# Kernel tuning notes

Measured on AMD Instinct MI355X. Metric: run time of the kernel, lower is better.

## Reference

```python
import jax, jax.numpy as jnp
import numpy as np

N_LOC = 20000
N_EXP = 200000
H = 64
E = 1500000
L = 400000


def setup_inputs() -> dict:
    key = jax.random.key(0)
    ks = jax.random.split(key, 24)
    f = jnp.float32
    w = lambda k, shp: jax.random.normal(k, shp, dtype=f) * 0.1
    # edges: ('location','of','experts'): src in [0,N_LOC), dst in [0,N_EXP)
    src = jax.random.randint(ks[0], (E,), 0, N_LOC)
    dst = jax.random.randint(ks[1], (E,), 0, N_EXP)
    edge_of = jnp.stack([src, dst])          # location -> experts
    edge_rev = jnp.stack([dst, src])         # experts -> location (ToUndirected)
    row = jax.random.randint(ks[2], (L,), 0, N_LOC)
    col = jax.random.randint(ks[3], (L,), 0, N_EXP)
    edge_label_index = jnp.stack([row, col])
    return dict(
        emb_loc=w(ks[4], (N_LOC, H)), emb_exp=w(ks[5], (N_EXP, H)),
        W1l_of=w(ks[6], (H, H)), b1_of=jnp.zeros((H,), f), W1r_of=w(ks[7], (H, H)),
        W1l_rev=w(ks[8], (H, H)), b1_rev=jnp.zeros((H,), f), W1r_rev=w(ks[9], (H, H)),
        W2l_of=w(ks[10], (H, H)), b2_of=jnp.zeros((H,), f), W2r_of=w(ks[11], (H, H)),
        W2l_rev=w(ks[12], (H, H)), b2_rev=jnp.zeros((H,), f), W2r_rev=w(ks[13], (H, H)),
        dW1=w(ks[14], (2 * H, H)), db1=jnp.zeros((H,), f),
        dW2=w(ks[15], (H, 1)), db2=jnp.zeros((1,), f),
        edge_of=edge_of, edge_rev=edge_rev, edge_label_index=edge_label_index,
    )


def _sage(x_src, x_dst, edge, Wl, b, Wr, n_dst):
    # PyG SAGEConv: lin_l(mean of neighbor msgs) + lin_r(x_dst); bias only in lin_l
    s, d = edge[0], edge[1]
    msg = x_src[s]                                   # [E, H] gather
    summed = jax.ops.segment_sum(msg, d, num_segments=n_dst)
    cnt = jax.ops.segment_sum(jnp.ones((edge.shape[1],), x_src.dtype), d, num_segments=n_dst)
    agg = summed / jnp.maximum(cnt, 1.0)[:, None]
    return agg @ Wl + b + x_dst @ Wr


def reference(emb_loc, emb_exp,
              W1l_of, b1_of, W1r_of, W1l_rev, b1_rev, W1r_rev,
              W2l_of, b2_of, W2r_of, W2l_rev, b2_rev, W2r_rev,
              dW1, db1, dW2, db2,
              edge_of, edge_rev, edge_label_index):
    # layer 1 (to_hetero: one conv per edge type; each dst type has one incoming type)
    z_exp = jax.nn.relu(_sage(emb_loc, emb_exp, edge_of, W1l_of, b1_of, W1r_of, N_EXP))
    z_loc = jax.nn.relu(_sage(emb_exp, emb_loc, edge_rev, W1l_rev, b1_rev, W1r_rev, N_LOC))
    # layer 2 (no relu)
    z_exp2 = _sage(z_loc, z_exp, edge_of, W2l_of, b2_of, W2r_of, N_EXP)
    z_loc2 = _sage(z_exp, z_loc, edge_rev, W2l_rev, b2_rev, W2r_rev, N_LOC)
    # EdgeDecoder: gather-concat-MLP
    row, col = edge_label_index[0], edge_label_index[1]
    z = jnp.concatenate([z_loc2[row], z_exp2[col]], axis=-1)  # [L, 2H]
    h = jax.nn.relu(z @ dW1 + db1)
    out = (h @ dW2 + db2).reshape(-1)
    return out
```

## Files before the change

kernel.cpp:

```cpp
#include <hip/hip_runtime.h>

#define H 64
#define NE 1500000
#define NLOC 20000
#define NEXP 200000
#define NL 400000
#define PAD_E 32
#define PAD_L 128

#define EB 896
#define NBE 224
#define LB 112
#define NBL 179
#define BIN_CHUNK 2048
#define NBIN ((NE + BIN_CHUNK - 1) / BIN_CHUNK)
#define EBSLOT 28
#define LBSLOT 32
#define ECAP 8192
#define LCAP 10240
#define FCAP 4096

#define WS_NEED 90546112ULL

typedef int vint4 __attribute__((ext_vector_type(4)));
typedef _Float16 f16x8 __attribute__((ext_vector_type(8)));
typedef _Float16 f16x4 __attribute__((ext_vector_type(4)));
typedef float f32x4 __attribute__((ext_vector_type(4)));
typedef unsigned int u32;
typedef unsigned short u16;
typedef unsigned long long u64;

__device__ __forceinline__ float bcastf(float v, int k) {
  return __int_as_float(__builtin_amdgcn_readlane(__float_as_int(v), k));
}
__device__ __forceinline__ int bcasti(int v, int k) {
  return __builtin_amdgcn_readlane(v, k);
}
__device__ __forceinline__ int sel4(int g, int n0, int n1, int n2, int n3) {
  return (g & 2) ? ((g & 1) ? n3 : n2) : ((g & 1) ? n1 : n0);
}

__global__ __launch_bounds__(256) void bin_kernel(
    const int* __restrict__ src, const int* __restrict__ dst,
    u32* __restrict__ expQ, u32* __restrict__ locQ,
    int* __restrict__ qcnt, int* __restrict__ flbk_cnt,
    u64* __restrict__ flbkQ)
{
  __shared__ u32 eb[NBE * EBSLOT];
  __shared__ u32 lb[NBL * LBSLOT];
  __shared__ int ec[NBE], lc[NBL], ebase[NBE], lbase[NBL];

  const int tid = threadIdx.x;
  for (int i = tid; i < NBE; i += 256) ec[i] = 0;
  for (int i = tid; i < NBL; i += 256) lc[i] = 0;
  __syncthreads();

  const long base = (long)blockIdx.x * BIN_CHUNK + tid * 8;
  if (base < NE) {
    vint4 s0 = __builtin_nontemporal_load((const vint4*)(src + base));
    vint4 s1 = __builtin_nontemporal_load((const vint4*)(src + base + 4));
    vint4 d0 = __builtin_nontemporal_load((const vint4*)(dst + base));
    vint4 d1 = __builtin_nontemporal_load((const vint4*)(dst + base + 4));
    int ss[8] = {s0.x, s0.y, s0.z, s0.w, s1.x, s1.y, s1.z, s1.w};
    int dd[8] = {d0.x, d0.y, d0.z, d0.w, d1.x, d1.y, d1.z, d1.w};
#pragma unroll
    for (int k = 0; k < 8; k++) {
      const u32 d = (u32)dd[k], s = (u32)ss[k];
      {
        const u32 b = d / (u32)EB;
        const int pos = atomicAdd(&ec[b], 1);
        if (pos < EBSLOT) {
          eb[b * EBSLOT + pos] = ((d - b * EB) << 16) | s;
        } else {
          int fi = atomicAdd(flbk_cnt, 1);
          if (fi < FCAP) flbkQ[fi] = ((u64)d << 32) | (u64)s;
        }
      }
      {
        const u32 b = s / (u32)LB;
        const int pos = atomicAdd(&lc[b], 1);
        if (pos < LBSLOT) {
          lb[b * LBSLOT + pos] = ((s - b * LB) << 18) | d;
        } else {
          int fi = atomicAdd(flbk_cnt, 1);
          if (fi < FCAP) flbkQ[fi] = (1ULL << 63) | ((u64)s << 32) | (u64)d;
        }
      }
    }
  }
  __syncthreads();

  for (int i = tid; i < NBE; i += 256) {
    const int c = min(ec[i], EBSLOT);
    ebase[i] = c ? atomicAdd(&qcnt[i], c) : 0;
  }
  for (int i = tid; i < NBL; i += 256) {
    const int c = min(lc[i], LBSLOT);
    lbase[i] = c ? atomicAdd(&qcnt[NBE + i], c) : 0;
  }
  __syncthreads();

  const int wid = tid >> 6, ln = tid & 63;
  for (int b = wid; b < NBE; b += 4) {
    const int c = min(ec[b], EBSLOT);
    if (ln < c) {
      const int idx = ebase[b] + ln;
      const u32 r = eb[b * EBSLOT + ln];
      if (idx < ECAP) {
        expQ[(long)b * ECAP + idx] = r;
      } else {
        int fi = atomicAdd(flbk_cnt, 1);
        if (fi < FCAP)
          flbkQ[fi] = ((u64)(b * EB + (r >> 16)) << 32) | (u64)(r & 0xFFFF);
      }
    }
  }
  for (int b = wid; b < NBL; b += 4) {
    const int c = min(lc[b], LBSLOT);
    if (ln < c) {
      const int idx = lbase[b] + ln;
      const u32 r = lb[b * LBSLOT + ln];
      if (idx < LCAP) {
        locQ[(long)b * LCAP + idx] = r;
      } else {
        int fi = atomicAdd(flbk_cnt, 1);
        if (fi < FCAP)
          flbkQ[fi] = (1ULL << 63) | ((u64)(b * LB + (r >> 18)) << 32) |
                      (u64)(r & 0x3FFFF);
      }
    }
  }
}

__global__ __launch_bounds__(256) void build_kernel(
    const u32* __restrict__ expQ, const u32* __restrict__ locQ,
    const int* __restrict__ qcnt,
    u16* __restrict__ nbr_exp, int* __restrict__ nbr_loc,
    int* __restrict__ cnt_exp, int* __restrict__ cnt_loc)
{
  __shared__ char ldsraw[60928];
  const int tid = threadIdx.x;
  if (blockIdx.x < NBE) {
    const int b = blockIdx.x;
    u16* rows = (u16*)ldsraw;
    int* cnts = (int*)(ldsraw + 57344);
    for (int i = tid; i < EB; i += 256) cnts[i] = 0;
    __syncthreads();
    const int n = min(qcnt[b], ECAP);
    for (int i = tid; i < n; i += 256) {
      const u32 r = expQ[(long)b * ECAP + i];
      const int nl = (int)(r >> 16);
      const int pos = atomicAdd(&cnts[nl], 1);
      if (pos < PAD_E) rows[nl * PAD_E + pos] = (u16)(r & 0xFFFF);
    }
    __syncthreads();
    const int node0 = b * EB;
    const int nn = min(EB, NEXP - node0);
    u32* grows = (u32*)(nbr_exp + (long)node0 * PAD_E);
    const u32* lrows = (const u32*)rows;
    for (int j = tid; j < nn * (PAD_E / 2); j += 256) grows[j] = lrows[j];
    for (int i = tid; i < nn; i += 256) cnt_exp[node0 + i] = cnts[i];
  } else {
    const int b = blockIdx.x - NBE;
    int* rows = (int*)ldsraw;
    int* cnts = (int*)(ldsraw + 57344);
    for (int i = tid; i < LB; i += 256) cnts[i] = 0;
    __syncthreads();
    const int n = min(qcnt[NBE + b], LCAP);
    for (int i = tid; i < n; i += 256) {
      const u32 r = locQ[(long)b * LCAP + i];
      const int sl = (int)(r >> 18);
      const int pos = atomicAdd(&cnts[sl], 1);
      if (pos < PAD_L) rows[sl * PAD_L + pos] = (int)(r & 0x3FFFF);
    }
    __syncthreads();
    const int node0 = b * LB;
    const int nn = min(LB, NLOC - node0);
    int* grows = nbr_loc + (long)node0 * PAD_L;
    for (int j = tid; j < nn * PAD_L; j += 256) grows[j] = rows[j];
    for (int i = tid; i < nn; i += 256) cnt_loc[node0 + i] = cnts[i];
  }
}

__global__ __launch_bounds__(256) void prep_kernel(
    const float* __restrict__ W2r_of, const float* __restrict__ W2l_of,
    const float* __restrict__ W2l_rev, const float* __restrict__ W2r_rev,
    const float* __restrict__ dW1, const float* __restrict__ b2_of,
    const float* __restrict__ b2_rev,
    float* __restrict__ Wf_q, float* __restrict__ Wf_y2,
    float* __restrict__ Wf_t2, float* __restrict__ Wf_p,
    float* __restrict__ bf_q, float* __restrict__ bf_p,
    const int* __restrict__ flbk_cnt, const u64* __restrict__ flbkQ,
    u16* __restrict__ nbr_exp, int* __restrict__ nbr_loc,
    int* __restrict__ cnt_exp, int* __restrict__ cnt_loc,
    const float* __restrict__ emb_loc, _Float16* __restrict__ Ylh,
    const float* __restrict__ W1l_of,
    const float* __restrict__ W1r_of, const float* __restrict__ W1l_rev,
    _Float16* __restrict__ W1rT16, _Float16* __restrict__ W1lrT16,
    _Float16* __restrict__ WfqT16, _Float16* __restrict__ Wft2T16)
{
  const int lane = threadIdx.x & 63;
  const int w = threadIdx.x >> 6;
  const float* dW1a = dW1;
  const float* dW1b = dW1 + H * H;
  if (blockIdx.x < 4) {
    const float* A; const float* B; float* C; _Float16* CT;
    switch (blockIdx.x) {
      case 0:  A = W2r_of;  B = dW1b; C = Wf_q;  CT = WfqT16;  break;
      case 1:  A = W2l_of;  B = dW1b; C = Wf_y2; CT = nullptr; break;
      case 2:  A = W2l_rev; B = dW1a; C = Wf_t2; CT = Wft2T16; break;
      default: A = W2r_rev; B = dW1a; C = Wf_p;  CT = nullptr; break;
    }
    float b[H];
#pragma unroll
    for (int k = 0; k < H; k++) b[k] = B[k * H + lane];
    for (int r = w * 16; r < w * 16 + 16; r++) {
      const float xv = A[r * H + lane];
      float a0 = 0.f, a1 = 0.f;
#pragma unroll
      for (int k = 0; k < H; k += 2) {
        a0 += bcastf(xv, k)     * b[k];
        a1 += bcastf(xv, k + 1) * b[k + 1];
      }
      const float val = a0 + a1;
      C[r * H + lane] = val;
      if (CT) CT[(long)lane * H + r] = (_Float16)val;
    }
  } else if (blockIdx.x == 4) {
    if (w < 2) {
      const float* bv_src = (w == 0) ? b2_of : b2_rev;
      const float* B      = (w == 0) ? dW1b  : dW1a;
      float* o            = (w == 0) ? bf_q  : bf_p;
      float wk[H];
#pragma unroll
      for (int k = 0; k < H; k++) wk[k] = B[k * H + lane];
      const float bv = bv_src[lane];
      float a = 0.f;
#pragma unroll
      for (int k = 0; k < H; k++) a += bcastf(bv, k) * wk[k];
      o[lane] = a;
    }
  } else if (blockIdx.x == 5) {
    const int n = min(*flbk_cnt, FCAP);
    for (int i = threadIdx.x; i < n; i += 256) {
      const u64 rec = flbkQ[i];
      const int node = (int)((rec >> 32) & 0x3FFFF);
      const int val  = (int)(rec & 0x3FFFF);
      if ((rec >> 63) == 0) {
        int pos = atomicAdd(&cnt_exp[node], 1);
        if (pos < PAD_E) nbr_exp[(long)node * PAD_E + pos] = (u16)val;
      } else {
        int pos = atomicAdd(&cnt_loc[node], 1);
        if (pos < PAD_L) nbr_loc[(long)node * PAD_L + pos] = val;
      }
    }
  } else if (blockIdx.x < 8) {
    const float* S = (blockIdx.x == 6) ? W1r_of : W1l_rev;
    _Float16* D    = (blockIdx.x == 6) ? W1rT16 : W1lrT16;
    for (int k = w * 16; k < w * 16 + 16; k++)
      D[(long)lane * H + k] = (_Float16)S[(long)k * H + lane];
  } else {
    float wreg[H];
#pragma unroll
    for (int k = 0; k < H; k++) wreg[k] = W1l_of[k * H + lane];
    const int gw2 = (blockIdx.x - 8) * 4 + w;
    for (int r = gw2; r < NLOC; r += 5000) {
      const float xv = emb_loc[(long)r * H + lane];
      float a0 = 0.f, a1 = 0.f;
#pragma unroll
      for (int k = 0; k < H; k += 2) {
        a0 += bcastf(xv, k)     * wreg[k];
        a1 += bcastf(xv, k + 1) * wreg[k + 1];
      }
      Ylh[(long)r * H + lane] = (_Float16)(a0 + a1);
    }
  }
}

__global__ __launch_bounds__(256, 4) void dense_linear_kernel(
    const float* __restrict__ x, _Float16* __restrict__ out16,
    const float* __restrict__ W, int n)
{
  const int lane = threadIdx.x & 63;
  const int gw = (blockIdx.x * 256 + threadIdx.x) >> 6;
  const int nw = (gridDim.x * 256) >> 6;
  float w[H];
#pragma unroll
  for (int k = 0; k < H; k++) w[k] = W[k * H + lane];
  for (int i = gw; i < n; i += nw) {
    const float xv = x[i * H + lane];
    float a0 = 0.f, a1 = 0.f;
#pragma unroll
    for (int k = 0; k < H; k += 2) {
      a0 += bcastf(xv, k)     * w[k];
      a1 += bcastf(xv, k + 1) * w[k + 1];
    }
    out16[i * H + lane] = (_Float16)(a0 + a1);
  }
}

__global__ __launch_bounds__(256, 4) void mfma_pass_kernel(
    const u16* __restrict__ nbr, const int* __restrict__ cnt,
    const _Float16* __restrict__ y,
    const float* a32, const _Float16* a16,
    _Float16* out1, const _Float16* __restrict__ W1T,
    const float* __restrict__ bias, int relu,
    _Float16* out2, const _Float16* __restrict__ W2T)
{
  const int w = threadIdx.x >> 6;
  const int lane = threadIdx.x & 63;
  const int q = lane >> 4;
  const int cidx = lane & 15;
  const int rb = blockIdx.x * 16;

  __shared__ float Gs[16 * 68];

  const _Float16* bt1 = W1T + (long)(w * 16 + cidx) * H;
  f16x8 b1lo = *(const f16x8*)(bt1 + q * 8);
  f16x8 b1hi = *(const f16x8*)(bt1 + 32 + q * 8);
  f16x8 b2lo, b2hi;
  if (out2) {
    const _Float16* bt2 = W2T + (long)(w * 16 + cidx) * H;
    b2lo = *(const f16x8*)(bt2 + q * 8);
    b2hi = *(const f16x8*)(bt2 + 32 + q * 8);
  }

  f16x8 a0, a1;
  if (a16) {
    const _Float16* ar = a16 + (long)(rb + cidx) * H;
    a0 = *(const f16x8*)(ar + q * 8);
    a1 = *(const f16x8*)(ar + 32 + q * 8);
  } else {
    const float* ar = a32 + (long)(rb + cidx) * H;
    f32x4 v0 = *(const f32x4*)(ar + q * 8);
    f32x4 v1 = *(const f32x4*)(ar + q * 8 + 4);
    f32x4 v2 = *(const f32x4*)(ar + 32 + q * 8);
    f32x4 v3 = *(const f32x4*)(ar + 32 + q * 8 + 4);
#pragma unroll
    for (int j = 0; j < 4; j++) {
      a0[j] = (_Float16)v0[j];
      a0[j + 4] = (_Float16)v1[j];
      a1[j] = (_Float16)v2[j];
      a1[j + 4] = (_Float16)v3[j];
    }
  }

  if (y) {
    const int i0r = rb + w * 4;
    const int g = lane >> 4;
    const int sub = lane & 15;
    int c4v[4];
#pragma unroll
    for (int rr = 0; rr < 4; rr++) c4v[rr] = cnt[i0r + rr];
    int id4[4];
#pragma unroll
    for (int rr = 0; rr < 4; rr++) {
      const int c = min(c4v[rr], PAD_E);
      id4[rr] = (lane < c) ? (int)nbr[(long)(i0r + rr) * PAD_E + lane] : 0;
    }
#pragma unroll
    for (int rr = 0; rr < 4; rr++) {
      const int cc = min(c4v[rr], PAD_E);
      const int id = id4[rr];
      const int kl = cc - 1;
      float s0 = 0.f, s1 = 0.f, s2 = 0.f, s3 = 0.f;
      for (int k = 0; k < cc; k += 4) {
        const int n0 = bcasti(id, k);
        const int n1 = bcasti(id, min(k + 1, kl));
        const int n2 = bcasti(id, min(k + 2, kl));
        const int n3 = bcasti(id, min(k + 3, kl));
        const int ns = sel4(g, n0, n1, n2, n3);
        const f16x4 v = *(const f16x4*)(y + (long)ns * H + sub * 4);
        const float msk = (k + g < cc) ? 1.0f : 0.0f;
        s0 = fmaf(msk, (float)v[0], s0);
        s1 = fmaf(msk, (float)v[1], s1);
        s2 = fmaf(msk, (float)v[2], s2);
        s3 = fmaf(msk, (float)v[3], s3);
      }
      s0 += __shfl_xor(s0, 16); s0 += __shfl_xor(s0, 32);
      s1 += __shfl_xor(s1, 16); s1 += __shfl_xor(s1, 32);
      s2 += __shfl_xor(s2, 16); s2 += __shfl_xor(s2, 32);
      s3 += __shfl_xor(s3, 16); s3 += __shfl_xor(s3, 32);
      const float inv = 1.0f / fmaxf((float)c4v[rr], 1.0f);
      if (lane < 16) {
        float* gp = &Gs[(w * 4 + rr) * 68 + 4 * lane];
        gp[0] = s0 * inv; gp[1] = s1 * inv;
        gp[2] = s2 * inv; gp[3] = s3 * inv;
      }
    }
  }

  f32x4 acc1 = {0.f, 0.f, 0.f, 0.f};
  acc1 = __builtin_amdgcn_mfma_f32_16x16x32_f16(a0, b1lo, acc1, 0, 0, 0);
  acc1 = __builtin_amdgcn_mfma_f32_16x16x32_f16(a1, b1hi, acc1, 0, 0, 0);
  f32x4 acc2 = {0.f, 0.f, 0.f, 0.f};
  if (out2) {
    acc2 = __builtin_amdgcn_mfma_f32_16x16x32_f16(a0, b2lo, acc2, 0, 0, 0);
    acc2 = __builtin_amdgcn_mfma_f32_16x16x32_f16(a1, b2hi, acc2, 0, 0, 0);
  }

  const float bj = bias ? bias[w * 16 + cidx] : 0.f;
  __syncthreads();
#pragma unroll
  for (int reg = 0; reg < 4; reg++) {
    const int r = q * 4 + reg;
    float v = acc1[reg] + bj;
    if (y) v += Gs[r * 68 + w * 16 + cidx];
    if (relu) v = fmaxf(v, 0.f);
    out1[(long)(rb + r) * H + w * 16 + cidx] = (_Float16)v;
    if (out2)
      out2[(long)(rb + r) * H + w * 16 + cidx] = (_Float16)acc2[reg];
  }
}

__global__ __launch_bounds__(256, 4) void loc_gather_kernel(
    const int* __restrict__ nbr, const int* __restrict__ cnt,
    const _Float16* __restrict__ T, const float* __restrict__ x,
    float* __restrict__ out32, _Float16* __restrict__ out16,
    const float* __restrict__ Wr, const float* __restrict__ bias,
    int n, int relu)
{
  const int lane = threadIdx.x & 63;
  const int gw = (blockIdx.x * 256 + threadIdx.x) >> 6;
  const int nw = (gridDim.x * 256) >> 6;
  const int g = lane >> 4;
  const int sub = lane & 15;
  float wr[H];
#pragma unroll
  for (int k = 0; k < H; k++) wr[k] = Wr[k * H + lane];
  const float bj = bias[lane];
  for (int i = gw; i < n; i += nw) {
    const int c = cnt[i];
    const int cc = min(c, PAD_L);
    const int* nb = nbr + (long)i * PAD_L;
    float s0 = 0.f, s1 = 0.f, s2 = 0.f, s3 = 0.f;
    float s4 = 0.f, s5 = 0.f, s6 = 0.f, s7 = 0.f;
    int e = 0;
    while (e < cc) {
      const int m = min(cc - e, 64);
      const int id = (lane < m) ? nb[e + lane] : 0;
      const int ml = m - 1;
      for (int k = 0; k < m; k += 8) {
        const int a0i = bcasti(id, k);
        const int a1i = bcasti(id, min(k + 1, ml));
        const int a2i = bcasti(id, min(k + 2, ml));
        const int a3i = bcasti(id, min(k + 3, ml));
        const int nsA = sel4(g, a0i, a1i, a2i, a3i);
        const f16x4 vA = *(const f16x4*)(T + (long)nsA * H + sub * 4);
        const int b0i = bcasti(id, min(k + 4, ml));
        const int b1i = bcasti(id, min(k + 5, ml));
        const int b2i = bcasti(id, min(k + 6, ml));
        const int b3i = bcasti(id, min(k + 7, ml));
        const int nsB = sel4(g, b0i, b1i, b2i, b3i);
        const f16x4 vB = *(const f16x4*)(T + (long)nsB * H + sub * 4);
        const float mA = (k + g < m) ? 1.0f : 0.0f;
        const float mB = (k + 4 + g < m) ? 1.0f : 0.0f;
        s0 = fmaf(mA, (float)vA[0], s0);
        s1 = fmaf(mA, (float)vA[1], s1);
        s2 = fmaf(mA, (float)vA[2], s2);
        s3 = fmaf(mA, (float)vA[3], s3);
        s4 = fmaf(mB, (float)vB[0], s4);
        s5 = fmaf(mB, (float)vB[1], s5);
        s6 = fmaf(mB, (float)vB[2], s6);
        s7 = fmaf(mB, (float)vB[3], s7);
      }
      e += m;
    }
    s0 += s4; s1 += s5; s2 += s6; s3 += s7;
    s0 += __shfl_xor(s0, 16); s0 += __shfl_xor(s0, 32);
    s1 += __shfl_xor(s1, 16); s1 += __shfl_xor(s1, 32);
    s2 += __shfl_xor(s2, 16); s2 += __shfl_xor(s2, 32);
    s3 += __shfl_xor(s3, 16); s3 += __shfl_xor(s3, 32);
    const int srcl = lane >> 2;
    const float v0 = __shfl(s0, srcl);
    const float v1 = __shfl(s1, srcl);
    const float v2 = __shfl(s2, srcl);
    const float v3 = __shfl(s3, srcl);
    const int r2 = lane & 3;
    const float sg = (r2 & 2) ? ((r2 & 1) ? v3 : v2) : ((r2 & 1) ? v1 : v0);
    const float agg = sg / fmaxf((float)c, 1.0f);
    const float xv = x[(long)i * H + lane];
    float a0 = 0.f, a1 = 0.f;
#pragma unroll
    for (int k = 0; k < H; k += 2) {
      a0 += bcastf(xv, k)     * wr[k];
      a1 += bcastf(xv, k + 1) * wr[k + 1];
    }
    float acc = agg + bj + a0 + a1;
    if (relu) acc = fmaxf(acc, 0.0f);
    if (out32) out32[(long)i * H + lane] = acc;
    else       out16[(long)i * H + lane] = (_Float16)acc;
  }
}

__global__ __launch_bounds__(256, 4) void edge_kernel(
    const int* __restrict__ row, const int* __restrict__ col,
    const _Float16* __restrict__ P, const _Float16* __restrict__ Q,
    const float* __restrict__ db1, const float* __restrict__ dW2,
    const float* __restrict__ db2, float* __restrict__ out)
{
  const int lane = threadIdx.x & 63;
  const int gw = (blockIdx.x * 256 + threadIdx.x) >> 6;
  const int nw = (gridDim.x * 256) >> 6;
  const int g = lane >> 4;
  const int sub = lane & 15;
  const f32x4 bj4 = *(const f32x4*)(db1 + 4 * sub);
  const f32x4 w24 = *(const f32x4*)(dW2 + 4 * sub);
  const float b2 = db2[0];
  for (int e = gw * 4; e < NL; e += nw * 4) {
    const int r0 = row[e], r1 = row[e + 1], r2i = row[e + 2], r3 = row[e + 3];
    const int c0 = col[e], c1 = col[e + 1], c2i = col[e + 2], c3 = col[e + 3];
    const int rs = sel4(g, r0, r1, r2i, r3);
    const int cs = sel4(g, c0, c1, c2i, c3);
    const f16x4 pv = *(const f16x4*)(P + (long)rs * H + sub * 4);
    const f16x4 qv = *(const f16x4*)(Q + (long)cs * H + sub * 4);
    float h = fmaxf((float)pv[0] + (float)qv[0] + bj4[0], 0.f) * w24[0]
            + fmaxf((float)pv[1] + (float)qv[1] + bj4[1], 0.f) * w24[1]
            + fmaxf((float)pv[2] + (float)qv[2] + bj4[2], 0.f) * w24[2]
            + fmaxf((float)pv[3] + (float)qv[3] + bj4[3], 0.f) * w24[3];
    h += __shfl_xor(h, 1);
    h += __shfl_xor(h, 2);
    h += __shfl_xor(h, 4);
    h += __shfl_xor(h, 8);
    if (sub == 0) out[e + g] = h + b2;
  }
}

extern "C" void kernel_launch(void* const* d_in, const int* in_sizes, int n_in,
                              void* d_out, int out_size, void* d_ws, size_t ws_size,
                              hipStream_t stream) {
  const float* emb_loc = (const float*)d_in[0];
  const float* emb_exp = (const float*)d_in[1];
  const float* W1l_of  = (const float*)d_in[2];
  const float* b1_of   = (const float*)d_in[3];
  const float* W1r_of  = (const float*)d_in[4];
  const float* W1l_rev = (const float*)d_in[5];
  const float* b1_rev  = (const float*)d_in[6];
  const float* W1r_rev = (const float*)d_in[7];
  const float* W2l_of  = (const float*)d_in[8];
  const float* b2_of   = (const float*)d_in[9];
  const float* W2r_of  = (const float*)d_in[10];
  const float* W2l_rev = (const float*)d_in[11];
  const float* b2_rev  = (const float*)d_in[12];
  const float* W2r_rev = (const float*)d_in[13];
  const float* dW1     = (const float*)d_in[14];
  const float* db1     = (const float*)d_in[15];
  const float* dW2     = (const float*)d_in[16];
  const float* db2     = (const float*)d_in[17];
  const int*   edge_of = (const int*)d_in[18];
  const int*   eli     = (const int*)d_in[20];

  const int* src = edge_of;
  const int* dst = edge_of + NE;
  const int* row = eli;
  const int* col = eli + NL;

  if (ws_size < WS_NEED) return;

  char* ws = (char*)d_ws;
  int*            cnt_loc = (int*)(ws);
  int*            cnt_exp = (int*)(ws + 80000);
  int*            nbr_loc = (int*)(ws + 880064);
  unsigned short* nbr_exp = (unsigned short*)(ws + 11120064);
  _Float16*       Ylh     = (_Float16*)(ws + 23920064);
  _Float16*       Y2fh    = (_Float16*)(ws + 26480064);
  float*          z_loc   = (float*)(ws + 29040064);
  _Float16*       PH      = (_Float16*)(ws + 34160064);
  _Float16*       W1rT16  = (_Float16*)(ws + 36720064);
  _Float16*       W1lrT16 = (_Float16*)(ws + 36728256);
  _Float16*       WfqT16  = (_Float16*)(ws + 36736448);
  _Float16*       Wft2T16 = (_Float16*)(ws + 36744640);
  _Float16*       ZE      = (_Float16*)(ws + 39280064);
  _Float16*       TH      = (_Float16*)(ws + 64880064);
  u32*            expQ    = (u32*)(ws + 64880064);
  u32*            locQ    = (u32*)(ws + 72220096);
  int*            qcnt    = (int*)(ws + 79551936);
  int*            flbk    = (int*)(ws + 79553552);
  u64*            flbkQ   = (u64*)(ws + 79554048);
  float*          Wf_q    = (float*)(ws + 90480064);
  float*          Wf_y2   = (float*)(ws + 90496448);
  float*          Wf_t2   = (float*)(ws + 90512832);
  float*          Wf_p    = (float*)(ws + 90529216);
  float*          bf_q    = (float*)(ws + 90545600);
  float*          bf_p    = (float*)(ws + 90545856);
  float*          out     = (float*)d_out;

  (void)hipMemsetAsync(ws + 79551936, 0, 2048, stream);

  bin_kernel<<<NBIN, 256, 0, stream>>>(src, dst, expQ, locQ, qcnt, flbk, flbkQ);
  build_kernel<<<NBE + NBL, 256, 0, stream>>>(expQ, locQ, qcnt,
      nbr_exp, nbr_loc, cnt_exp, cnt_loc);
  prep_kernel<<<1258, 256, 0, stream>>>(W2r_of, W2l_of, W2l_rev, W2r_rev,
                                        dW1, b2_of, b2_rev,
                                        Wf_q, Wf_y2, Wf_t2, Wf_p, bf_q, bf_p,
                                        flbk, flbkQ, nbr_exp, nbr_loc,
                                        cnt_exp, cnt_loc,
                                        emb_loc, Ylh, W1l_of,
                                        W1r_of, W1l_rev,
                                        W1rT16, W1lrT16, WfqT16, Wft2T16);

  mfma_pass_kernel<<<NEXP / 16, 256, 0, stream>>>(nbr_exp, cnt_exp, Ylh,
      emb_exp, (const _Float16*)nullptr, ZE, W1rT16, b1_of, 1, TH, W1lrT16);
  loc_gather_kernel<<<2048, 256, 0, stream>>>(nbr_loc, cnt_loc, TH,
      emb_loc, z_loc, (_Float16*)nullptr, W1r_rev, b1_rev, NLOC, 1);

  dense_linear_kernel<<<1280, 256, 0, stream>>>(z_loc, Y2fh, Wf_y2, NLOC);
  mfma_pass_kernel<<<NEXP / 16, 256, 0, stream>>>(nbr_exp, cnt_exp, Y2fh,
      (const float*)nullptr, ZE, ZE, WfqT16, bf_q, 0, TH, Wft2T16);
  loc_gather_kernel<<<2048, 256, 0, stream>>>(nbr_loc, cnt_loc, TH,
      z_loc, (float*)nullptr, PH, Wf_p, bf_p, NLOC, 0);

  edge_kernel<<<2048, 256, 0, stream>>>(row, col, PH, ZE,
                                        db1, dW2, db2, out);
}
```

Measured before the change: 501.5 us.

## Fuse both location-side gather passes into one kernel using ZE directly

Merges the two loc_gather passes into a single kernel. It gathers TH and the layer-1 expert embeddings ZE at the same time and computes the layer-2 location projection (ZE aggregate times Wt2 plus z times Wp) in place, so the second mfma pass no longer writes TH. This removes one kernel launch and a full re-read of the neighbour lists, and the weights move from per-thread registers into fp16 shared memory. In exchange, each gather step now loads two rows, weights are held in fp16, and each node does more serial FMAs.

```diff
diff --git a/kernel.cpp b/kernel.cpp
--- a/kernel.cpp
+++ b/kernel.cpp
@@ -196,20 +196,24 @@
     const float* __restrict__ emb_loc, _Float16* __restrict__ Ylh,
     const float* __restrict__ W1l_of,
     const float* __restrict__ W1r_of, const float* __restrict__ W1l_rev,
+    const float* __restrict__ W1r_rev,
     _Float16* __restrict__ W1rT16, _Float16* __restrict__ W1lrT16,
-    _Float16* __restrict__ WfqT16, _Float16* __restrict__ Wft2T16)
+    _Float16* __restrict__ WfqT16,
+    _Float16* __restrict__ W1rRevH16, _Float16* __restrict__ Wt2H16,
+    _Float16* __restrict__ WpH16)
 {
   const int lane = threadIdx.x & 63;
   const int w = threadIdx.x >> 6;
   const float* dW1a = dW1;
   const float* dW1b = dW1 + H * H;
   if (blockIdx.x < 4) {
-    const float* A; const float* B; float* C; _Float16* CT;
+    const float* A; const float* B; float* C;
+    _Float16* CT; _Float16* CH;
     switch (blockIdx.x) {
-      case 0:  A = W2r_of;  B = dW1b; C = Wf_q;  CT = WfqT16;  break;
-      case 1:  A = W2l_of;  B = dW1b; C = Wf_y2; CT = nullptr; break;
-      case 2:  A = W2l_rev; B = dW1a; C = Wf_t2; CT = Wft2T16; break;
-      default: A = W2r_rev; B = dW1a; C = Wf_p;  CT = nullptr; break;
+      case 0:  A = W2r_of;  B = dW1b; C = Wf_q;  CT = WfqT16; CH = nullptr; break;
+      case 1:  A = W2l_of;  B = dW1b; C = Wf_y2; CT = nullptr; CH = nullptr; break;
+      case 2:  A = W2l_rev; B = dW1a; C = Wf_t2; CT = nullptr; CH = Wt2H16; break;
+      default: A = W2r_rev; B = dW1a; C = Wf_p;  CT = nullptr; CH = WpH16;  break;
     }
     float b[H];
 #pragma unroll
@@ -225,6 +229,7 @@
       const float val = a0 + a1;
       C[r * H + lane] = val;
       if (CT) CT[(long)lane * H + r] = (_Float16)val;
+      if (CH) CH[(long)r * H + lane] = (_Float16)val;
     }
   } else if (blockIdx.x == 4) {
     if (w < 2) {
@@ -259,11 +264,14 @@
     _Float16* D    = (blockIdx.x == 6) ? W1rT16 : W1lrT16;
     for (int k = w * 16; k < w * 16 + 16; k++)
       D[(long)lane * H + k] = (_Float16)S[(long)k * H + lane];
+  } else if (blockIdx.x == 8) {
+    for (int k = w * 16; k < w * 16 + 16; k++)
+      W1rRevH16[(long)k * H + lane] = (_Float16)W1r_rev[(long)k * H + lane];
   } else {
     float wreg[H];
 #pragma unroll
     for (int k = 0; k < H; k++) wreg[k] = W1l_of[k * H + lane];
-    const int gw2 = (blockIdx.x - 8) * 4 + w;
+    const int gw2 = (blockIdx.x - 9) * 4 + w;
     for (int r = gw2; r < NLOC; r += 5000) {
       const float xv = emb_loc[(long)r * H + lane];
       float a0 = 0.f, a1 = 0.f;
@@ -413,83 +421,100 @@
   }
 }
 
-__global__ __launch_bounds__(256, 4) void loc_gather_kernel(
+__global__ __launch_bounds__(256, 4) void fused_loc_kernel(
     const int* __restrict__ nbr, const int* __restrict__ cnt,
-    const _Float16* __restrict__ T, const float* __restrict__ x,
-    float* __restrict__ out32, _Float16* __restrict__ out16,
-    const float* __restrict__ Wr, const float* __restrict__ bias,
-    int n, int relu)
+    const _Float16* __restrict__ T1, const _Float16* __restrict__ ZEt,
+    const float* __restrict__ x,
+    float* __restrict__ z_out, _Float16* __restrict__ ph_out,
+    const _Float16* __restrict__ Wr16, const _Float16* __restrict__ Wt216,
+    const _Float16* __restrict__ Wp16,
+    const float* __restrict__ b1, const float* __restrict__ bfp)
 {
-  const int lane = threadIdx.x & 63;
-  const int gw = (blockIdx.x * 256 + threadIdx.x) >> 6;
+  __shared__ _Float16 Wl[3 * 4096];
+  const int tid = threadIdx.x;
+  for (int j = tid * 8; j < 4096; j += 2048) {
+    *(f16x8*)&Wl[j]        = *(const f16x8*)&Wr16[j];
+    *(f16x8*)&Wl[4096 + j] = *(const f16x8*)&Wt216[j];
+    *(f16x8*)&Wl[8192 + j] = *(const f16x8*)&Wp16[j];
+  }
+  __syncthreads();
+
+  const int lane = tid & 63;
+  const int gw = (blockIdx.x * 256 + tid) >> 6;
   const int nw = (gridDim.x * 256) >> 6;
   const int g = lane >> 4;
   const int sub = lane & 15;
-  float wr[H];
-#pragma unroll
-  for (int k = 0; k < H; k++) wr[k] = Wr[k * H + lane];
-  const float bj = bias[lane];
-  for (int i = gw; i < n; i += nw) {
+  const float bj = b1[lane];
+  const float bp = bfp[lane];
+  for (int i = gw; i < NLOC; i += nw) {
     const int c = cnt[i];
     const int cc = min(c, PAD_L);
     const int* nb = nbr + (long)i * PAD_L;
-    float s0 = 0.f, s1 = 0.f, s2 = 0.f, s3 = 0.f;
-    float s4 = 0.f, s5 = 0.f, s6 = 0.f, s7 = 0.f;
+    float t0 = 0.f, t1 = 0.f, t2 = 0.f, t3 = 0.f;
+    float u0 = 0.f, u1 = 0.f, u2 = 0.f, u3 = 0.f;
     int e = 0;
     while (e < cc) {
       const int m = min(cc - e, 64);
       const int id = (lane < m) ? nb[e + lane] : 0;
       const int ml = m - 1;
-      for (int k = 0; k < m; k += 8) {
-        const int a0i = bcasti(id, k);
-        const int a1i = bcasti(id, min(k + 1, ml));
-        const int a2i = bcasti(id, min(k + 2, ml));
-        const int a3i = bcasti(id, min(k + 3, ml));
-        const int nsA = sel4(g, a0i, a1i, a2i, a3i);
-        const f16x4 vA = *(const f16x4*)(T + (long)nsA * H + sub * 4);
-        const int b0i = bcasti(id, min(k + 4, ml));
-        const int b1i = bcasti(id, min(k + 5, ml));
-        const int b2i = bcasti(id, min(k + 6, ml));
-        const int b3i = bcasti(id, min(k + 7, ml));
-        const int nsB = sel4(g, b0i, b1i, b2i, b3i);
-        const f16x4 vB = *(const f16x4*)(T + (long)nsB * H + sub * 4);
-        const float mA = (k + g < m) ? 1.0f : 0.0f;
-        const float mB = (k + 4 + g < m) ? 1.0f : 0.0f;
-        s0 = fmaf(mA, (float)vA[0], s0);
-        s1 = fmaf(mA, (float)vA[1], s1);
-        s2 = fmaf(mA, (float)vA[2], s2);
-        s3 = fmaf(mA, (float)vA[3], s3);
-        s4 = fmaf(mB, (float)vB[0], s4);
-        s5 = fmaf(mB, (float)vB[1], s5);
-        s6 = fmaf(mB, (float)vB[2], s6);
-        s7 = fmaf(mB, (float)vB[3], s7);
+      for (int k = 0; k < m; k += 4) {
+        const int n0 = bcasti(id, k);
+        const int n1 = bcasti(id, min(k + 1, ml));
+        const int n2 = bcasti(id, min(k + 2, ml));
+        const int n3 = bcasti(id, min(k + 3, ml));
+        const int ns = sel4(g, n0, n1, n2, n3);
+        const long ro = (long)ns * H + sub * 4;
+        const f16x4 vT = *(const f16x4*)(T1 + ro);
+        const f16x4 vZ = *(const f16x4*)(ZEt + ro);
+        const float mk = (k + g < m) ? 1.0f : 0.0f;
+        t0 = fmaf(mk, (float)vT[0], t0);
+        t1 = fmaf(mk, (float)vT[1], t1);
+        t2 = fmaf(mk, (float)vT[2], t2);
+        t3 = fmaf(mk, (float)vT[3], t3);
+        u0 = fmaf(mk, (float)vZ[0], u0);
+        u1 = fmaf(mk, (float)vZ[1], u1);
+        u2 = fmaf(mk, (float)vZ[2], u2);
+        u3 = fmaf(mk, (float)vZ[3], u3);
       }
       e += m;
     }
-    s0 += s4; s1 += s5; s2 += s6; s3 += s7;
-    s0 += __shfl_xor(s0, 16); s0 += __shfl_xor(s0, 32);
-    s1 += __shfl_xor(s1, 16); s1 += __shfl_xor(s1, 32);
-    s2 += __shfl_xor(s2, 16); s2 += __shfl_xor(s2, 32);
-    s3 += __shfl_xor(s3, 16); s3 += __shfl_xor(s3, 32);
+    t0 += __shfl_xor(t0, 16); t0 += __shfl_xor(t0, 32);
+    t1 += __shfl_xor(t1, 16); t1 += __shfl_xor(t1, 32);
+    t2 += __shfl_xor(t2, 16); t2 += __shfl_xor(t2, 32);
+    t3 += __shfl_xor(t3, 16); t3 += __shfl_xor(t3, 32);
+    u0 += __shfl_xor(u0, 16); u0 += __shfl_xor(u0, 32);
+    u1 += __shfl_xor(u1, 16); u1 += __shfl_xor(u1, 32);
+    u2 += __shfl_xor(u2, 16); u2 += __shfl_xor(u2, 32);
+    u3 += __shfl_xor(u3, 16); u3 += __shfl_xor(u3, 32);
     const int srcl = lane >> 2;
-    const float v0 = __shfl(s0, srcl);
-    const float v1 = __shfl(s1, srcl);
-    const float v2 = __shfl(s2, srcl);
-    const float v3 = __shfl(s3, srcl);
     const int r2 = lane & 3;
-    const float sg = (r2 & 2) ? ((r2 & 1) ? v3 : v2) : ((r2 & 1) ? v1 : v0);
-    const float agg = sg / fmaxf((float)c, 1.0f);
+    const float vt0 = __shfl(t0, srcl), vt1 = __shfl(t1, srcl);
+    const float vt2 = __shfl(t2, srcl), vt3 = __shfl(t3, srcl);
+    const float vu0 = __shfl(u0, srcl), vu1 = __shfl(u1, srcl);
+    const float vu2 = __shfl(u2, srcl), vu3 = __shfl(u3, srcl);
+    const float inv = 1.0f / fmaxf((float)c, 1.0f);
+    const float g1 = ((r2 & 2) ? ((r2 & 1) ? vt3 : vt2)
+                               : ((r2 & 1) ? vt1 : vt0)) * inv;
+    const float gz = ((r2 & 2) ? ((r2 & 1) ? vu3 : vu2)
+                               : ((r2 & 1) ? vu1 : vu0)) * inv;
     const float xv = x[(long)i * H + lane];
     float a0 = 0.f, a1 = 0.f;
 #pragma unroll
     for (int k = 0; k < H; k += 2) {
-      a0 += bcastf(xv, k)     * wr[k];
-      a1 += bcastf(xv, k + 1) * wr[k + 1];
-    }
-    float acc = agg + bj + a0 + a1;
-    if (relu) acc = fmaxf(acc, 0.0f);
-    if (out32) out32[(long)i * H + lane] = acc;
-    else       out16[(long)i * H + lane] = (_Float16)acc;
+      a0 = fmaf(bcastf(xv, k),     (float)Wl[k * H + lane], a0);
+      a1 = fmaf(bcastf(xv, k + 1), (float)Wl[(k + 1) * H + lane], a1);
+    }
+    const float z = fmaxf(g1 + bj + a0 + a1, 0.0f);
+    z_out[(long)i * H + lane] = z;
+    float p0 = 0.f, p1 = 0.f;
+#pragma unroll
+    for (int k = 0; k < H; k += 2) {
+      p0 = fmaf(bcastf(gz, k),     (float)Wl[4096 + k * H + lane], p0);
+      p0 = fmaf(bcastf(z, k),      (float)Wl[8192 + k * H + lane], p0);
+      p1 = fmaf(bcastf(gz, k + 1), (float)Wl[4096 + (k + 1) * H + lane], p1);
+      p1 = fmaf(bcastf(z, k + 1),  (float)Wl[8192 + (k + 1) * H + lane], p1);
+    }
+    ph_out[(long)i * H + lane] = (_Float16)(p0 + p1 + bp);
   }
 }
 
@@ -569,7 +594,9 @@
   _Float16*       W1rT16  = (_Float16*)(ws + 36720064);
   _Float16*       W1lrT16 = (_Float16*)(ws + 36728256);
   _Float16*       WfqT16  = (_Float16*)(ws + 36736448);
-  _Float16*       Wft2T16 = (_Float16*)(ws + 36744640);
+  _Float16*       W1rRevH16 = (_Float16*)(ws + 36752832);
+  _Float16*       Wt2H16  = (_Float16*)(ws + 36761024);
+  _Float16*       WpH16   = (_Float16*)(ws + 36769216);
   _Float16*       ZE      = (_Float16*)(ws + 39280064);
   _Float16*       TH      = (_Float16*)(ws + 64880064);
   u32*            expQ    = (u32*)(ws + 64880064);
@@ -590,26 +617,24 @@
   bin_kernel<<<NBIN, 256, 0, stream>>>(src, dst, expQ, locQ, qcnt, flbk, flbkQ);
   build_kernel<<<NBE + NBL, 256, 0, stream>>>(expQ, locQ, qcnt,
       nbr_exp, nbr_loc, cnt_exp, cnt_loc);
-  prep_kernel<<<1258, 256, 0, stream>>>(W2r_of, W2l_of, W2l_rev, W2r_rev,
+  prep_kernel<<<1259, 256, 0, stream>>>(W2r_of, W2l_of, W2l_rev, W2r_rev,
                                         dW1, b2_of, b2_rev,
                                         Wf_q, Wf_y2, Wf_t2, Wf_p, bf_q, bf_p,
                                         flbk, flbkQ, nbr_exp, nbr_loc,
                                         cnt_exp, cnt_loc,
                                         emb_loc, Ylh, W1l_of,
-                                        W1r_of, W1l_rev,
-                                        W1rT16, W1lrT16, WfqT16, Wft2T16);
+                                        W1r_of, W1l_rev, W1r_rev,
+                                        W1rT16, W1lrT16, WfqT16,
+                                        W1rRevH16, Wt2H16, WpH16);
 
   mfma_pass_kernel<<<NEXP / 16, 256, 0, stream>>>(nbr_exp, cnt_exp, Ylh,
       emb_exp, (const _Float16*)nullptr, ZE, W1rT16, b1_of, 1, TH, W1lrT16);
-  loc_gather_kernel<<<2048, 256, 0, stream>>>(nbr_loc, cnt_loc, TH,
-      emb_loc, z_loc, (_Float16*)nullptr, W1r_rev, b1_rev, NLOC, 1);
-
+  fused_loc_kernel<<<2048, 256, 0, stream>>>(nbr_loc, cnt_loc, TH, ZE,
+      emb_loc, z_loc, PH, W1rRevH16, Wt2H16, WpH16, b1_rev, bf_p);
   dense_linear_kernel<<<1280, 256, 0, stream>>>(z_loc, Y2fh, Wf_y2, NLOC);
   mfma_pass_kernel<<<NEXP / 16, 256, 0, stream>>>(nbr_exp, cnt_exp, Y2fh,
-      (const float*)nullptr, ZE, ZE, WfqT16, bf_q, 0, TH, Wft2T16);
-  loc_gather_kernel<<<2048, 256, 0, stream>>>(nbr_loc, cnt_loc, TH,
-      z_loc, (float*)nullptr, PH, Wf_p, bf_p, NLOC, 0);
-
+      (const float*)nullptr, ZE, ZE, WfqT16, bf_q, 0,
+      (_Float16*)nullptr, (const _Float16*)nullptr);
   edge_kernel<<<2048, 256, 0, stream>>>(row, col, PH, ZE,
                                         db1, dW2, db2, out);
 }
```

New measurement: 597.7 us. 19.2% more time.
